# Kernel optimization log

Hardware: AMD Instinct MI355X
Metric: run time of the kernel (lower is better)

## Reference

```python
import jax, jax.numpy as jnp
import numpy as np
import math

B, S, C, H = 32, 500, 1024, 16
D = C // H  # head dim = 64

def setup_inputs() -> dict:
    key = jax.random.key(0)
    ks = jax.random.split(key, 9)
    sc = 1.0 / math.sqrt(C)
    return {
        "x": jax.random.normal(ks[0], (B, S, C), dtype=jnp.float32),
        "Wq": jax.random.normal(ks[1], (C, C), dtype=jnp.float32) * sc,
        "bq": jnp.zeros((C,), dtype=jnp.float32),
        "Wk": jax.random.normal(ks[2], (C, C), dtype=jnp.float32) * sc,
        "bk": jnp.zeros((C,), dtype=jnp.float32),
        "Wv": jax.random.normal(ks[3], (C, C), dtype=jnp.float32) * sc,
        "bv": jnp.zeros((C,), dtype=jnp.float32),
        "Wp": jax.random.normal(ks[4], (C, C), dtype=jnp.float32) * sc,
        "bp": jnp.zeros((C,), dtype=jnp.float32),
    }

def reference(x, Wq, bq, Wk, bk, Wv, bv, Wp, bp):
    # Projections -> [B, H, S, D]
    q = (x @ Wq + bq).reshape(B, S, H, D).transpose(0, 2, 1, 3)
    k = (x @ Wk + bk).reshape(B, S, H, D).transpose(0, 2, 1, 3)
    v = (x @ Wv + bv).reshape(B, S, H, D).transpose(0, 2, 1, 3)
    # Scaled scores [B, H, S, S]
    att = jnp.einsum('bhqd,bhkd->bhqk', q, k) * (1.0 / math.sqrt(D))
    causal = jnp.tril(jnp.ones((S, S), dtype=bool))
    att = jnp.where(causal[None, None], att, jnp.float32(-1e10))
    att = jax.nn.softmax(att, axis=-1)
    # (dropout is identity in eval mode)
    y = jnp.einsum('bhqk,bhkd->bhqd', att, v)  # [B, H, S, D]
    y = y.transpose(0, 2, 1, 3).reshape(B, S, C)
    return y @ Wp + bp
```

## Files before the change

### kernel.cpp

```cpp
#include <hip/hip_runtime.h>
#include <math.h>

#define B_ 32
#define S_ 500
#define C_ 1024
#define H_ 16
#define D_ 64
#define M_ (B_ * S_)
#define MP 16128
#define SP 512

typedef _Float16 f16;
typedef f16 f16x8 __attribute__((ext_vector_type(8)));
typedef f16 f16x4 __attribute__((ext_vector_type(4)));
typedef float f32x4 __attribute__((ext_vector_type(4)));

#define GLOBAL_AS __attribute__((address_space(1)))
#define LDS_AS __attribute__((address_space(3)))

__device__ __forceinline__ void async_load16(const void* g, void* l) {
    __builtin_amdgcn_global_load_lds((const GLOBAL_AS void*)g, (LDS_AS void*)l, 16, 0, 0);
}
template <int N>
__device__ __forceinline__ void wait_vmcnt() {
    asm volatile("s_waitcnt vmcnt(%0)" ::"i"(N) : "memory");
}

struct MaskF { static constexpr bool value = false; };
struct MaskT { static constexpr bool value = true; };

__global__ __launch_bounds__(256) void prep(
    const float* __restrict__ x, f16* __restrict__ xf, int n8_real, int n8_tot,
    const float* __restrict__ W0, const float* __restrict__ W1,
    const float* __restrict__ W2, const float* __restrict__ W3,
    f16* __restrict__ T0, f16* __restrict__ T1,
    f16* __restrict__ T2, f16* __restrict__ T3)
{
    __shared__ float t[32][33];
    const int bid = blockIdx.x;
    const int tid = threadIdx.x;
    if (bid < 4096) {
        const int z = bid >> 10, rem = bid & 1023;
        const float* W = (z == 0) ? W0 : (z == 1) ? W1 : (z == 2) ? W2 : W3;
        f16* T = (z == 0) ? T0 : (z == 1) ? T1 : (z == 2) ? T2 : T3;
        const int n0 = (rem & 31) * 32, k0 = (rem >> 5) * 32;
        const int tx = tid & 31, ty = tid >> 5;
#pragma unroll
        for (int i = 0; i < 4; ++i)
            t[ty + 8 * i][tx] = W[(size_t)(k0 + ty + 8 * i) * C_ + n0 + tx];
        __syncthreads();
#pragma unroll
        for (int i = 0; i < 4; ++i) {
            int n = ty + 8 * i;
            T[(size_t)(n0 + n) * C_ + k0 + tx] = (f16)t[tx][n];
        }
    } else {
        int i = (bid - 4096) * 256 + tid;
        if (i >= n8_tot) return;
        f16x8 h;
        if (i < n8_real) {
            float4 a = ((const float4*)x)[2 * i];
            float4 b = ((const float4*)x)[2 * i + 1];
            h[0] = (f16)a.x; h[1] = (f16)a.y; h[2] = (f16)a.z; h[3] = (f16)a.w;
            h[4] = (f16)b.x; h[5] = (f16)b.y; h[6] = (f16)b.z; h[7] = (f16)b.w;
        } else {
            f16 z8 = (f16)0.f;
            h[0] = z8; h[1] = z8; h[2] = z8; h[3] = z8;
            h[4] = z8; h[5] = z8; h[6] = z8; h[7] = z8;
        }
        ((f16x8*)xf)[i] = h;
    }
}

#define BAR()                          \
    __builtin_amdgcn_s_barrier();      \
    __builtin_amdgcn_sched_barrier(0)

#define LD_A(MH)                                                              \
    _Pragma("unroll") for (int i = 0; i < 4; ++i)                             \
    _Pragma("unroll") for (int ks = 0; ks < 2; ++ks)                          \
        af[i][ks] = *(const f16x8*)(smem + c * 32768 + (MH) * 8192 +          \
                                    rA_off + i * 1024 + sw[ks]);

#define LD_B(NH)                                                              \
    _Pragma("unroll") for (int j = 0; j < 2; ++j)                             \
    _Pragma("unroll") for (int ks = 0; ks < 2; ++ks)                          \
        bf[NH][j][ks] = *(const f16x8*)(smem + c * 32768 + 16384 +            \
                                        (NH) * 8192 + rB_off + j * 1024 +     \
                                        sw[ks]);

#define MMA(MH, NH)                                                           \
    __builtin_amdgcn_s_setprio(1);                                            \
    _Pragma("unroll") for (int i = 0; i < 4; ++i)                             \
    _Pragma("unroll") for (int j = 0; j < 2; ++j)                             \
    _Pragma("unroll") for (int ks = 0; ks < 2; ++ks)                          \
        acc[(MH) * 4 + i][(NH) * 2 + j] =                                     \
            __builtin_amdgcn_mfma_f32_16x16x32_f16(                           \
                af[i][ks], bf[NH][j][ks], acc[(MH) * 4 + i][(NH) * 2 + j],    \
                0, 0, 0);                                                     \
    __builtin_amdgcn_s_setprio(0)

template <int MODE>
__global__ __launch_bounds__(512) void gemm256(
    const f16* __restrict__ A, const f16* __restrict__ W,
    const float* __restrict__ b0, const float* __restrict__ b1,
    const float* __restrict__ b2, void* __restrict__ o0,
    void* __restrict__ o1, void* __restrict__ o2)
{
    constexpr int K = C_;
    constexpr int NB = (MODE == 0) ? 12 : 4;
    constexpr int NWG = 63 * NB;
    constexpr int Q8 = NWG / 8, R8 = NWG % 8;
    extern __shared__ __align__(16) f16 smem[];

    const int tid = threadIdx.x;
    const int lane = tid & 63, w = tid >> 6;
    const int wm = w >> 2, wn = w & 3;
    const int quad = lane >> 4, lr = lane & 15;

    const int lin = blockIdx.x;
    const int xcd = lin & 7, pos = lin >> 3;
    const int wg = (xcd < R8 ? xcd * (Q8 + 1) : R8 * (Q8 + 1) + (xcd - R8) * Q8) + pos;
    const int m0 = (wg / NB) * 256;
    const int n0 = (wg % NB) * 256;

    const int srow = tid >> 3;
    const int gc8 = (tid & 7) ^ (srow & 7);
    const f16* pAt = A + (size_t)(m0 + srow) * K + gc8 * 8;
    const f16* pBt = W + (size_t)(n0 + (srow & 31) + ((srow >> 5) << 6)) * K + gc8 * 8;
    f16* dA = smem + tid * 8;
    f16* dB = smem + 16384 + tid * 8;

    auto stageA = [&](int kt, int cb, int h) __attribute__((always_inline)) {
        const f16* s = pAt + (size_t)(h * 64) * K + kt * 64;
        f16* d = dA + cb * 32768 + h * 8192;
        async_load16(s, d);
        async_load16(s + (size_t)128 * K, d + 4096);
    };
    auto stageB = [&](int kt, int cb, int h) __attribute__((always_inline)) {
        const f16* s = pBt + (size_t)(h * 32) * K + kt * 64;
        f16* d = dB + cb * 32768 + h * 8192;
        async_load16(s, d);
        async_load16(s + (size_t)128 * K, d + 4096);
    };

    int sw[2];
    sw[0] = ((0 + quad) ^ (lr & 7)) * 8;
    sw[1] = ((4 + quad) ^ (lr & 7)) * 8;
    const int rA_off = (wm * 64 + lr) * 64;
    const int rB_off = (wn * 32 + lr) * 64;

    f32x4 acc[8][4];
#pragma unroll
    for (int i = 0; i < 8; ++i)
#pragma unroll
        for (int j = 0; j < 4; ++j) acc[i][j] = (f32x4)0.f;
    f16x8 af[4][2], bf[2][2][2];

    stageA(0, 0, 0); stageB(0, 0, 0); stageB(0, 0, 1); stageA(0, 0, 1);

    constexpr int NT = K / 64;
    for (int kt = 0; kt < NT - 1; ++kt) {
        const int c = kt & 1, nb = c ^ 1;
        stageA(kt + 1, nb, 0);
        wait_vmcnt<6>(); BAR();
        LD_A(0); LD_B(0);
        MMA(0, 0);
        stageB(kt + 1, nb, 0);
        wait_vmcnt<6>(); BAR();
        LD_B(1);
        MMA(0, 1);
        stageB(kt + 1, nb, 1);
        wait_vmcnt<6>(); BAR();
        LD_A(1);
        MMA(1, 1);
        stageA(kt + 1, nb, 1);
        MMA(1, 0);
    }
    {
        const int c = (NT - 1) & 1;
        wait_vmcnt<4>(); BAR();
        LD_A(0); LD_B(0);
        MMA(0, 0);
        wait_vmcnt<2>(); BAR();
        LD_B(1);
        MMA(0, 1);
        wait_vmcnt<0>(); BAR();
        LD_A(1);
        MMA(1, 1);
        MMA(1, 0);
    }

#pragma unroll
    for (int nf = 0; nf < 4; ++nf) {
        int gcn = n0 + wn * 64 + nf * 16 + lr;
        if (MODE == 1) {
            float bv = b0[gcn];
            float* of = (float*)o0;
#pragma unroll
            for (int mf = 0; mf < 8; ++mf) {
                int gr0 = m0 + wm * 128 + mf * 16 + quad * 4;
                if (gr0 >= M_) continue;
#pragma unroll
                for (int r = 0; r < 4; ++r)
                    of[(size_t)(gr0 + r) * C_ + gcn] = acc[mf][nf][r] + bv;
            }
        } else {
            int sec = gcn >> 10;
            int gcl = gcn & 1023;
            const float* bp = (sec == 0) ? b0 : (sec == 1) ? b1 : b2;
            float bv = bp[gcl];
            float osc = (sec == 0) ? 0.125f : 1.0f;
            int h = gcl >> 6, d = gcl & 63;
#pragma unroll
            for (int mf = 0; mf < 8; ++mf) {
                int gr0 = m0 + wm * 128 + mf * 16 + quad * 4;
                if (gr0 >= M_) continue;
                int b = gr0 / S_, s0 = gr0 - b * S_;
                if (sec < 2) {
                    f16* oq = (f16*)((sec == 0) ? o0 : o1);
#pragma unroll
                    for (int r = 0; r < 4; ++r) {
                        float v = (acc[mf][nf][r] + bv) * osc;
                        size_t idx = (((size_t)b * H_ + h) * S_ + (s0 + r)) * D_ + d;
                        oq[idx] = (f16)v;
                    }
                } else {
                    f16* ov = (f16*)o2;
                    f16x4 pk;
#pragma unroll
                    for (int r = 0; r < 4; ++r) pk[r] = (f16)(acc[mf][nf][r] + bv);
                    *(f16x4*)(ov + (((size_t)b * H_ + h) * D_ + d) * SP + s0) = pk;
                }
            }
        }
    }
}

__global__ __launch_bounds__(256) void attn_mfma(
    const f16* __restrict__ qg, const f16* __restrict__ kg,
    const f16* __restrict__ vt, f16* __restrict__ Y)
{
    __shared__ __align__(16) f16 sK[64 * 64];
    __shared__ __align__(16) f16 sVt[64 * 64];
    __shared__ __align__(16) f16 sP[4 * 32 * 64];

    const int tid = threadIdx.x;
    const int lin = blockIdx.x;
    const int xcd = lin & 7;
    const int pos = lin >> 3;
    const int bh = xcd * 64 + (pos >> 2);
    const int qt = 3 - (pos & 3);
    const int q0 = qt * 128;
    const int lane = tid & 63, w = tid >> 6;
    const int quad = lane >> 4, lr = lane & 15;
    const size_t gbase = (size_t)bh * S_ * D_;
    const size_t vbase = (size_t)bh * D_ * SP;
    const int psw = (lr & 7) << 1;

    f16x8 qf[2][2];
#pragma unroll
    for (int t = 0; t < 2; ++t) {
        int q = q0 + w * 32 + t * 16 + lr;
        const f16* pq = qg + gbase + (size_t)q * D_;
#pragma unroll
        for (int s2 = 0; s2 < 2; ++s2)
            qf[t][s2] = *(const f16x8*)(pq + quad * 8 + 32 * s2);
    }

    f32x4 accO[2][4];
#pragma unroll
    for (int t = 0; t < 2; ++t)
#pragma unroll
        for (int nt = 0; nt < 4; ++nt) accO[t][nt] = (f32x4)0.f;
    float l_run[2] = {0.f, 0.f};

    auto iter = [&](int kt, auto masked_tag) __attribute__((always_inline)) {
        constexpr bool MASKED = decltype(masked_tag)::value;
        const int k0 = kt * 64;
#pragma unroll
        for (int it = 0; it < 2; ++it) {
            int idx = it * 256 + tid;
            int row = idx >> 3, c = idx & 7;
            int csw = (c ^ (row & 7)) * 8;
            async_load16(kg + gbase + (size_t)(k0 + row) * D_ + csw, &sK[idx * 8]);
            async_load16(vt + vbase + (size_t)row * SP + k0 + csw, &sVt[idx * 8]);
        }
        __syncthreads();

        f32x4 accS[4][2];
#pragma unroll
        for (int mt = 0; mt < 4; ++mt)
#pragma unroll
            for (int t = 0; t < 2; ++t) accS[mt][t] = (f32x4)0.f;
        __builtin_amdgcn_s_setprio(1);
#pragma unroll
        for (int mt = 0; mt < 4; ++mt) {
            int row = mt * 16 + lr;
#pragma unroll
            for (int s2 = 0; s2 < 2; ++s2) {
                int off = row * 64 + (((quad + 4 * s2) ^ (lr & 7)) << 3);
                f16x8 ka = *(const f16x8*)&sK[off];
#pragma unroll
                for (int t = 0; t < 2; ++t)
                    accS[mt][t] = __builtin_amdgcn_mfma_f32_16x16x32_f16(
                        ka, qf[t][s2], accS[mt][t], 0, 0, 0);
            }
        }
        __builtin_amdgcn_s_setprio(0);

        float ls[2] = {0.f, 0.f};
#pragma unroll
        for (int mt = 0; mt < 4; ++mt)
#pragma unroll
            for (int t = 0; t < 2; ++t) {
                f16x4 pk;
#pragma unroll
                for (int r = 0; r < 4; ++r) {
                    float s = accS[mt][t][r];
                    if (MASKED) {
                        int key = k0 + mt * 16 + quad * 4 + r;
                        int qq = q0 + w * 32 + t * 16 + lr;
                        s = (key <= qq && key < S_) ? s : -1e30f;
                    }
                    float p = __expf(s);
                    ls[t] += p;
                    pk[r] = (f16)p;
                }
                int c8 = (mt * 4 + quad) ^ psw;
                *(f16x4*)&sP[w * 2048 + (t * 16 + lr) * 64 + c8 * 4] = pk;
            }
        ls[0] += __shfl_xor(ls[0], 16); ls[0] += __shfl_xor(ls[0], 32);
        ls[1] += __shfl_xor(ls[1], 16); ls[1] += __shfl_xor(ls[1], 32);
        l_run[0] += ls[0];
        l_run[1] += ls[1];

        __builtin_amdgcn_s_setprio(1);
#pragma unroll
        for (int t = 0; t < 2; ++t) {
            int pb = w * 2048 + (t * 16 + lr) * 64;
#pragma unroll
            for (int s2 = 0; s2 < 2; ++s2) {
                int c8 = (quad * 2 + 8 * s2) ^ psw;
                f16x8 pf = *(const f16x8*)&sP[pb + c8 * 4];
#pragma unroll
                for (int nt = 0; nt < 4; ++nt) {
                    f16x8 vf = *(const f16x8*)
                        &sVt[(nt * 16 + lr) * 64 + (((quad + 4 * s2) ^ (lr & 7)) << 3)];
                    accO[t][nt] = __builtin_amdgcn_mfma_f32_16x16x32_f16(
                        pf, vf, accO[t][nt], 0, 0, 0);
                }
            }
        }
        __builtin_amdgcn_s_setprio(0);
        __syncthreads();
    };

    for (int kt = 0; kt < 2 * qt; ++kt) iter(kt, MaskF{});
    iter(2 * qt, MaskT{});
    iter(2 * qt + 1, MaskT{});

    const int b = bh >> 4, h = bh & 15;
#pragma unroll
    for (int t = 0; t < 2; ++t) {
#pragma unroll
        for (int r = 0; r < 4; ++r) {
            float lsum = __shfl(l_run[t], quad * 4 + r);
            float iv = 1.f / lsum;
            int s = q0 + w * 32 + t * 16 + quad * 4 + r;
            if (s >= S_) continue;
            size_t rowbase = (size_t)(b * S_ + s) * C_ + h * 64;
#pragma unroll
            for (int nt = 0; nt < 4; ++nt)
                Y[rowbase + nt * 16 + lr] = (f16)(accO[t][nt][r] * iv);
        }
    }
}

extern "C" void kernel_launch(void* const* d_in, const int* in_sizes, int n_in,
                              void* d_out, int out_size, void* d_ws, size_t ws_size,
                              hipStream_t stream)
{
    const float* x = (const float*)d_in[0];
    const float* Wq = (const float*)d_in[1];
    const float* bq = (const float*)d_in[2];
    const float* Wk = (const float*)d_in[3];
    const float* bk = (const float*)d_in[4];
    const float* Wv = (const float*)d_in[5];
    const float* bv = (const float*)d_in[6];
    const float* Wp = (const float*)d_in[7];
    const float* bp = (const float*)d_in[8];

    const size_t NEL = (size_t)M_ * C_;
    const size_t WEL = (size_t)C_ * C_;
    f16* qf = (f16*)d_ws;
    f16* kf = qf + NEL;
    f16* vtw = kf + NEL;
    f16* xf = vtw + (size_t)B_ * H_ * D_ * SP;
    f16* wpf = xf + (size_t)MP * C_;
    f16* yf = xf;

    f16* wq = (f16*)d_out;
    f16* wk = wq + WEL;
    f16* wv = wk + WEL;

    hipFuncSetAttribute(reinterpret_cast<const void*>(&gemm256<0>),
                        hipFuncAttributeMaxDynamicSharedMemorySize, 131072);
    hipFuncSetAttribute(reinterpret_cast<const void*>(&gemm256<1>),
                        hipFuncAttributeMaxDynamicSharedMemorySize, 131072);

    int n8r = (int)(NEL / 8);
    int n8t = (int)((size_t)MP * C_ / 8);
    int nprep = 4096 + (n8t + 255) / 256;
    prep<<<nprep, 256, 0, stream>>>(x, xf, n8r, n8t,
                                    Wq, Wk, Wv, Wp, wq, wk, wv, wpf);

    gemm256<0><<<756, 512, 131072, stream>>>(xf, wq, bq, bk, bv, qf, kf, vtw);

    attn_mfma<<<2048, 256, 0, stream>>>(qf, kf, vtw, yf);

    gemm256<1><<<252, 512, 131072, stream>>>(yf, wpf, bp, nullptr, nullptr,
                                             d_out, nullptr, nullptr);
}
```

Measured before the change: 363.9 us.

## Double-buffer K/V tiles in attention kernel to overlap loads with MFMA

Doubles the LDS buffers for the K and V^T tiles and issues the async global-to-LDS loads for the next key tile before computing on the current one. It then waits on vmcnt so only the current tile's loads are complete. This hides global memory latency behind the QK and PV matrix-core work instead of stalling at a barrier every iteration. It costs extra LDS per block, which may lower occupancy, and adds two barriers per step.

```diff
diff --git a/kernel.cpp b/kernel.cpp
--- a/kernel.cpp
+++ b/kernel.cpp
@@ -241,8 +241,8 @@
     const f16* __restrict__ qg, const f16* __restrict__ kg,
     const f16* __restrict__ vt, f16* __restrict__ Y)
 {
-    __shared__ __align__(16) f16 sK[64 * 64];
-    __shared__ __align__(16) f16 sVt[64 * 64];
+    __shared__ __align__(16) f16 sK[2][64 * 64];
+    __shared__ __align__(16) f16 sVt[2][64 * 64];
     __shared__ __align__(16) f16 sP[4 * 32 * 64];
 
     const int tid = threadIdx.x;
@@ -275,18 +275,33 @@
         for (int nt = 0; nt < 4; ++nt) accO[t][nt] = (f32x4)0.f;
     float l_run[2] = {0.f, 0.f};
 
-    auto iter = [&](int kt, auto masked_tag) __attribute__((always_inline)) {
-        constexpr bool MASKED = decltype(masked_tag)::value;
+    const int NT = 2 * qt + 2;
+
+    auto stage = [&](int kt, int buf) __attribute__((always_inline)) {
         const int k0 = kt * 64;
 #pragma unroll
         for (int it = 0; it < 2; ++it) {
             int idx = it * 256 + tid;
             int row = idx >> 3, c = idx & 7;
             int csw = (c ^ (row & 7)) * 8;
-            async_load16(kg + gbase + (size_t)(k0 + row) * D_ + csw, &sK[idx * 8]);
-            async_load16(vt + vbase + (size_t)row * SP + k0 + csw, &sVt[idx * 8]);
-        }
-        __syncthreads();
+            async_load16(kg + gbase + (size_t)(k0 + row) * D_ + csw, &sK[buf][idx * 8]);
+            async_load16(vt + vbase + (size_t)row * SP + k0 + csw, &sVt[buf][idx * 8]);
+        }
+    };
+
+    auto step = [&](int kt, auto masked_tag) __attribute__((always_inline)) {
+        constexpr bool MASKED = decltype(masked_tag)::value;
+        const int cur = kt & 1;
+        const int k0 = kt * 64;
+
+        BAR();
+        if (kt + 1 < NT) {
+            stage(kt + 1, cur ^ 1);
+            wait_vmcnt<4>();
+        } else {
+            wait_vmcnt<0>();
+        }
+        BAR();
 
         f32x4 accS[4][2];
 #pragma unroll
@@ -300,7 +315,7 @@
 #pragma unroll
             for (int s2 = 0; s2 < 2; ++s2) {
                 int off = row * 64 + (((quad + 4 * s2) ^ (lr & 7)) << 3);
-                f16x8 ka = *(const f16x8*)&sK[off];
+                f16x8 ka = *(const f16x8*)&sK[cur][off];
 #pragma unroll
                 for (int t = 0; t < 2; ++t)
                     accS[mt][t] = __builtin_amdgcn_mfma_f32_16x16x32_f16(
@@ -346,19 +361,19 @@
 #pragma unroll
                 for (int nt = 0; nt < 4; ++nt) {
                     f16x8 vf = *(const f16x8*)
-                        &sVt[(nt * 16 + lr) * 64 + (((quad + 4 * s2) ^ (lr & 7)) << 3)];
+                        &sVt[cur][(nt * 16 + lr) * 64 + (((quad + 4 * s2) ^ (lr & 7)) << 3)];
                     accO[t][nt] = __builtin_amdgcn_mfma_f32_16x16x32_f16(
                         pf, vf, accO[t][nt], 0, 0, 0);
                 }
             }
         }
         __builtin_amdgcn_s_setprio(0);
-        __syncthreads();
     };
 
-    for (int kt = 0; kt < 2 * qt; ++kt) iter(kt, MaskF{});
-    iter(2 * qt, MaskT{});
-    iter(2 * qt + 1, MaskT{});
+    stage(0, 0);
+    for (int kt = 0; kt < 2 * qt; ++kt) step(kt, MaskF{});
+    step(2 * qt, MaskT{});
+    step(2 * qt + 1, MaskT{});
 
     const int b = bh >> 4, h = bh & 15;
 #pragma unroll
```

After: 358.2 us. About the same (-1.6%).
